# Optimization experiments

Hardware: AMD Instinct MI355X
Metric: run time of the kernel (lower is better)

Reference implementation:

```python
import jax, jax.numpy as jnp
import numpy as np

TOPK = 80
RADIUS_GAIN = 14.0
RADIUS_MIN = 1.5
RADIUS_MAX = 18.0
EPS = 1e-6


def _norm01(x, eps=EPS):
    # per-batch min/max normalization over all non-batch dims
    b = x.shape[0]
    flat = x.reshape(b, -1)
    mn = flat.min(axis=1).reshape(b, 1, 1, 1)
    mx = flat.max(axis=1).reshape(b, 1, 1, 1)
    return (x - mn) / (mx - mn + eps)


def _avg_pool(x, k):
    # torch avg_pool2d(kernel=k, stride=1, padding=k//2, count_include_pad=True)
    s = jax.lax.reduce_window(x, 0.0, jax.lax.add, (1, 1, k, k), (1, 1, 1, 1), 'SAME')
    return s / float(k * k)


def _max_pool(x, k):
    return jax.lax.reduce_window(x, -jnp.inf, jax.lax.max, (1, 1, k, k), (1, 1, 1, 1), 'SAME')


def _compact_connected_prior(score_map):
    occ = (score_map > 0.2).astype(score_map.dtype)
    local_occ = _avg_pool(occ, 9)
    local_mass = _avg_pool(score_map, 9)
    compact = _norm01(local_occ * local_mass)
    return score_map * compact


def _gaussian_map(score_map, depth):
    b, _, h, w = score_map.shape
    dtype = score_map.dtype
    pooled = _max_pool(score_map, 5)
    maxima = score_map * (score_map == pooled).astype(dtype)  # NMS keep local maxima

    flat = maxima.reshape(b, h * w)
    vals, inds = jax.lax.top_k(flat, TOPK)              # [B,K]
    vals = jnp.where(vals > 0, vals, jnp.zeros_like(vals))  # zero-weight masked peaks

    ys = (inds // w).astype(dtype)                       # [B,K]
    xs = (inds % w).astype(dtype)
    z = jnp.take_along_axis(depth.reshape(b, h * w), inds, axis=1)
    z = jnp.maximum(z, 1e-3)
    radius = jnp.clip(RADIUS_GAIN / z, RADIUS_MIN, RADIUS_MAX)
    sigma2 = (0.6 * radius) ** 2                         # [B,K]

    yy = jnp.arange(h, dtype=dtype)
    xx = jnp.arange(w, dtype=dtype)
    dx2 = (xx[None, None, None, :] - xs[:, :, None, None]) ** 2   # [B,K,1,W]
    dy2 = (yy[None, None, :, None] - ys[:, :, None, None]) ** 2   # [B,K,H,1]
    maps = vals[:, :, None, None] * jnp.exp(
        -(dx2 + dy2) / (2.0 * sigma2[:, :, None, None] + 1e-6))    # [B,K,H,W]
    gauss = maps.max(axis=1)[:, None]                    # [B,1,H,W]; maps>=0 so zero baseline preserved
    return _norm01(gauss)


def setup_inputs() -> dict:
    key = jax.random.key(0)
    k1, k2 = jax.random.split(key)
    B, H, W = 8, 320, 320
    voxel_score_map = jax.random.uniform(k1, (B, 1, H, W), dtype=jnp.float32)
    # depth within the module's valid z range [0.3, 20.0]
    depth = 0.3 + 19.7 * jax.random.uniform(k2, (B, 1, H, W), dtype=jnp.float32)
    return {'voxel_score_map': voxel_score_map, 'depth': depth}


def reference(voxel_score_map, depth):
    compact_score = _compact_connected_prior(voxel_score_map)
    return _gaussian_map(compact_score, depth)
```

## Files before the change

kernel.cpp:

```cpp
#include <hip/hip_runtime.h>
#include <math.h>

#define HH 320
#define WW 320
#define HWP (HH * WW)
#define KTOP 80
#define CNT_STRIDE 64
#define CAP (HWP / 2)
#define LVCAP 8192
#define TW 32
#define TH 64
#define NTPRX (WW / TW)
#define NTPI (NTPRX * (HH / TH))
#define GSW 64
#define GSH 16
#define SPRX (WW / GSW)
#define SPI (SPRX * (HH / GSH))
#define LOG2E 1.4426950408889634f
#define NLOG2TAU 19.931568569324174f

__device__ __forceinline__ void wave_minmax(float& mn, float& mx) {
    for (int off = 32; off > 0; off >>= 1) {
        mn = fminf(mn, __shfl_xor(mn, off, 64));
        mx = fmaxf(mx, __shfl_xor(mx, off, 64));
    }
}

__global__ __launch_bounds__(256) void pool_fused_k(
        const float* __restrict__ score, float* __restrict__ prod,
        float2* __restrict__ pmm, int* __restrict__ cand_cnt, int B_) {
    int tid = threadIdx.x;
    if (blockIdx.x == 0)
        for (int t = tid; t < B_ * CNT_STRIDE; t += 256) cand_cnt[t] = 0;
    int blk = blockIdx.x;
    int b = blk / NTPI, t = blk % NTPI;
    int ty0 = (t / NTPRX) * TH, tx0 = (t % NTPRX) * TW;
    __shared__ float rss[TH + 8][TW + 4];
    __shared__ float rso[TH + 8][TW + 4];
    const float4* img4 = (const float4*)(score + b * HWP);
    for (int i = tid; i < (TH + 8) * (TW / 4); i += 256) {
        int r = i / (TW / 4), q = i % (TW / 4);
        int gy = ty0 - 4 + r;
        float o0=0,o1=0,o2=0,o3=0,p0=0,p1=0,p2=0,p3=0;
        if (gy >= 0 && gy < HH) {
            const float4* row4 = img4 + gy * (WW / 4);
            int gq = tx0 / 4 + q;
            float4 a = (gq > 0) ? row4[gq - 1] : make_float4(0,0,0,0);
            float4 bb = row4[gq];
            float4 c = (gq < WW / 4 - 1) ? row4[gq + 1] : make_float4(0,0,0,0);
            float w0=a.x,w1=a.y,w2=a.z,w3=a.w,w4=bb.x,w5=bb.y,w6=bb.z,w7=bb.w,w8=c.x,w9=c.y,w10=c.z,w11=c.w;
            float s = w0+w1+w2+w3+w4+w5+w6+w7+w8;
            o0=s; s+=w9-w0; o1=s; s+=w10-w1; o2=s; s+=w11-w2; o3=s;
            float c0=(w0>0.2f)?1.f:0.f, c1=(w1>0.2f)?1.f:0.f, c2=(w2>0.2f)?1.f:0.f, c3=(w3>0.2f)?1.f:0.f;
            float c4=(w4>0.2f)?1.f:0.f, c5=(w5>0.2f)?1.f:0.f, c6=(w6>0.2f)?1.f:0.f, c7=(w7>0.2f)?1.f:0.f;
            float c8=(w8>0.2f)?1.f:0.f, c9=(w9>0.2f)?1.f:0.f, c10=(w10>0.2f)?1.f:0.f, c11=(w11>0.2f)?1.f:0.f;
            float u = c0+c1+c2+c3+c4+c5+c6+c7+c8;
            p0=u; u+=c9-c0; p1=u; u+=c10-c1; p2=u; u+=c11-c2; p3=u;
        }
        *(float4*)&rss[r][q * 4] = make_float4(o0,o1,o2,o3);
        *(float4*)&rso[r][q * 4] = make_float4(p0,p1,p2,p3);
    }
    __syncthreads();
    float tmn = INFINITY, tmx = 0.f;
    const float inv81 = 1.0f / 81.0f;
    float4* pr4 = (float4*)(prod + b * HWP);
    for (int i = tid; i < TH * (TW / 4); i += 256) {
        int r = i / (TW / 4), q = i % (TW / 4);
        float sx=0,sy=0,sz=0,sw=0, ox=0,oy=0,oz=0,ow=0;
#pragma unroll
        for (int j = 0; j < 9; ++j) {
            float4 s = *(float4*)&rss[r + j][q * 4];
            float4 o = *(float4*)&rso[r + j][q * 4];
            sx+=s.x; sy+=s.y; sz+=s.z; sw+=s.w;
            ox+=o.x; oy+=o.y; oz+=o.z; ow+=o.w;
        }
        float px=(ox*inv81)*(sx*inv81), py=(oy*inv81)*(sy*inv81);
        float pz=(oz*inv81)*(sz*inv81), pw=(ow*inv81)*(sw*inv81);
        pr4[(ty0 + r) * (WW / 4) + tx0 / 4 + q] = make_float4(px,py,pz,pw);
        tmn = fminf(tmn, fminf(fminf(px,py), fminf(pz,pw)));
        tmx = fmaxf(tmx, fmaxf(fmaxf(px,py), fmaxf(pz,pw)));
    }
    wave_minmax(tmn, tmx);
    __shared__ float wmn[4], wmx[4];
    int w = tid >> 6;
    if ((tid & 63) == 0) { wmn[w] = tmn; wmx[w] = tmx; }
    __syncthreads();
    if (tid == 0)
        pmm[blk] = make_float2(fminf(fminf(wmn[0],wmn[1]), fminf(wmn[2],wmn[3])),
                               fmaxf(fmaxf(wmx[0],wmx[1]), fmaxf(wmx[2],wmx[3])));
}

__global__ __launch_bounds__(256) void cs_nms_k(
        const float* __restrict__ score, const float* __restrict__ prod,
        const float2* __restrict__ pmm, float* __restrict__ cand_base,
        int* __restrict__ cand_cnt) {
    int tid = threadIdx.x;
    int blk = blockIdx.x;
    int b = blk / NTPI, t = blk % NTPI;
    int ty0 = (t / NTPRX) * TH, tx0 = (t % NTPRX) * TW;
    float tmn = INFINITY, tmx = 0.f;
    if (tid < NTPI) { float2 e = pmm[b * NTPI + tid]; tmn = e.x; tmx = e.y; }
    wave_minmax(tmn, tmx);
    __shared__ float s_mn, s_inv;
    if (tid == 0) { s_mn = tmn; s_inv = 1.0f / (tmx - tmn + 1e-6f); }
    __shared__ float cs[TH + 4][TW + 8 + 4];
    __shared__ float rm[TH + 4][TW + 4];
    __syncthreads();
    float mn = s_mn, inv = s_inv;
    const float4* sc4 = (const float4*)(score + b * HWP);
    const float4* pr4 = (const float4*)(prod + b * HWP);
    for (int i = tid; i < (TH + 4) * 10; i += 256) {
        int r = i / 10, q = i % 10;
        int gy = ty0 - 2 + r;
        int gq = tx0 / 4 - 1 + q;
        float4 c4 = make_float4(0,0,0,0);
        if (gy >= 0 && gy < HH && gq >= 0 && gq < WW / 4) {
            float4 s4 = sc4[gy * (WW / 4) + gq];
            float4 p4 = pr4[gy * (WW / 4) + gq];
            c4.x = s4.x * ((p4.x - mn) * inv); c4.y = s4.y * ((p4.y - mn) * inv);
            c4.z = s4.z * ((p4.z - mn) * inv); c4.w = s4.w * ((p4.w - mn) * inv);
        }
        *(float4*)&cs[r][q * 4] = c4;
    }
    __syncthreads();
    for (int i = tid; i < (TH + 4) * (TW / 4); i += 256) {
        int r = i / (TW / 4), x = (i % (TW / 4)) * 4;
        float c0=cs[r][x+2], c1=cs[r][x+3], c2=cs[r][x+4], c3=cs[r][x+5];
        float c4v=cs[r][x+6], c5=cs[r][x+7], c6=cs[r][x+8], c7=cs[r][x+9];
        float m01=fmaxf(c0,c1), m23=fmaxf(c2,c3), m45=fmaxf(c4v,c5), m67=fmaxf(c6,c7);
        float r0 = fmaxf(fmaxf(m01, m23), c4v);
        float r1 = fmaxf(fmaxf(c1, m23), m45);
        float r2 = fmaxf(fmaxf(m23, m45), c6);
        float r3 = fmaxf(fmaxf(c3, m45), m67);
        *(float4*)&rm[r][x] = make_float4(r0,r1,r2,r3);
    }
    __syncthreads();
    bool cd[8]; float vv[8]; int pb[2]; int offs[8];
#pragma unroll
    for (int qq = 0; qq < 2; ++qq) {
        int quad = qq * 256 + tid;
        int r = quad >> 3, x = (quad & 7) * 4;
        float4 v = *(float4*)&cs[r + 2][x + 4];
        float4 nm = *(float4*)&rm[r][x];
#pragma unroll
        for (int k = 1; k <= 4; ++k) {
            float4 rr = *(float4*)&rm[r + k][x];
            nm.x=fmaxf(nm.x,rr.x); nm.y=fmaxf(nm.y,rr.y);
            nm.z=fmaxf(nm.z,rr.z); nm.w=fmaxf(nm.w,rr.w);
        }
        pb[qq] = (ty0 + r) * WW + tx0 + x;
        cd[qq*4+0] = v.x > 0.f && v.x >= nm.x; vv[qq*4+0] = v.x;
        cd[qq*4+1] = v.y > 0.f && v.y >= nm.y; vv[qq*4+1] = v.y;
        cd[qq*4+2] = v.z > 0.f && v.z >= nm.z; vv[qq*4+2] = v.z;
        cd[qq*4+3] = v.w > 0.f && v.w >= nm.w; vv[qq*4+3] = v.w;
    }
    int lane = tid & 63, w = tid >> 6;
    unsigned long long lower = (1ULL << lane) - 1ULL;
    int wave_run = 0;
#pragma unroll
    for (int j = 0; j < 8; ++j) {
        unsigned long long m = __ballot(cd[j]);
        offs[j] = wave_run + __popcll(m & lower);
        wave_run += __popcll(m);
    }
    __shared__ int wbase[4];
    __shared__ int blockbase;
    if (lane == 0) wbase[w] = wave_run;
    __syncthreads();
    if (tid == 0) {
        int a0=wbase[0], a1=wbase[1], a2=wbase[2], a3=wbase[3];
        int tot = a0+a1+a2+a3;
        wbase[0]=0; wbase[1]=a0; wbase[2]=a0+a1; wbase[3]=a0+a1+a2;
        blockbase = tot ? atomicAdd(&cand_cnt[b * CNT_STRIDE], tot) : 0;
    }
    __syncthreads();
    float* cv = cand_base + b * HWP;
    int* ci = (int*)(cand_base + b * HWP + CAP);
    int bb2 = blockbase + wbase[w];
#pragma unroll
    for (int j = 0; j < 8; ++j) {
        if (cd[j]) {
            int slot = bb2 + offs[j];
            if (slot < CAP) { cv[slot] = vv[j]; ci[slot] = pb[j >> 2] + (j & 3); }
        }
    }
}

__global__ __launch_bounds__(1024) void topk_k(
        const float* __restrict__ cand_base, const int* __restrict__ cand_cnt,
        const float* __restrict__ depth, float4* __restrict__ pk4g) {
    int b = blockIdx.x;
    int tid = threadIdx.x;
    int n = cand_cnt[b * CNT_STRIDE];
    if (n > CAP) n = CAP;
    const float* cv = cand_base + b * HWP;
    const int* ci = (const int*)(cand_base + b * HWP + CAP);

    __shared__ float cvl[LVCAP];
    __shared__ int hist[256];
    __shared__ unsigned s_prefix;
    __shared__ int s_kth;
    __shared__ float sel_v[KTOP];
    __shared__ int sel_i[KTOP];
    __shared__ int s_ng, s_nt;
    __shared__ int tie_i[512];
    __shared__ float s_lvoff;

    bool inl = (n <= LVCAP);
    if (inl) {
        int n4 = n >> 2;
        const float4* cv4 = (const float4*)cv;
        for (int i = tid; i < n4; i += 1024) {
            float4 v = cv4[i];
            cvl[i*4+0] = v.x; cvl[i*4+1] = v.y; cvl[i*4+2] = v.z; cvl[i*4+3] = v.w;
        }
        for (int i = n4 * 4 + tid; i < n; i += 1024) cvl[i] = cv[i];
    }
    if (tid == 0) { s_prefix = 0; s_kth = KTOP; s_ng = 0; s_nt = 0; }
    if (tid < KTOP) { sel_v[tid] = 0.f; sel_i[tid] = -1; }
    __syncthreads();

    if (n > KTOP) {
        for (int shift = 24; shift >= 0; shift -= 8) {
            if (tid < 256) hist[tid] = 0;
            __syncthreads();
            unsigned pref = s_prefix;
            unsigned hmask = (shift == 24) ? 0u : (0xFFFFFFFFu << (shift + 8));
            for (int i = tid; i < n; i += 1024) {
                unsigned u = __float_as_uint(inl ? cvl[i] : cv[i]);
                if ((u & hmask) == (pref & hmask))
                    atomicAdd(&hist[(u >> shift) & 255], 1);
            }
            __syncthreads();
            if (tid < 64) {
                int h0 = hist[tid*4+0], h1 = hist[tid*4+1], h2 = hist[tid*4+2], h3 = hist[tid*4+3];
                int ls3 = h3, ls2 = h2 + ls3, ls1 = h1 + ls2, ls0 = h0 + ls1;
                int sum = ls0;
                for (int off = 1; off < 64; off <<= 1) {
                    int vv2 = __shfl_down(sum, off, 64);
                    if (tid + off < 64) sum += vv2;
                }
                int excl = sum - ls0;
                int kth = s_kth;
                int SS0=ls0+excl, SS1=ls1+excl, SS2=ls2+excl, SS3=ls3+excl, SS4=excl;
                unsigned pr = s_prefix;
                int bin = -1, rem = 0;
                if (SS0 >= kth && SS1 < kth) { bin = tid*4+0; rem = kth - SS1; }
                else if (SS1 >= kth && SS2 < kth) { bin = tid*4+1; rem = kth - SS2; }
                else if (SS2 >= kth && SS3 < kth) { bin = tid*4+2; rem = kth - SS3; }
                else if (SS3 >= kth && SS4 < kth) { bin = tid*4+3; rem = kth - SS4; }
                if (bin >= 0) { s_prefix = pr | ((unsigned)bin << shift); s_kth = rem; }
            }
            __syncthreads();
        }
        unsigned T = s_prefix;
        int need_eq = s_kth;
        for (int i = tid; i < n; i += 1024) {
            unsigned u = __float_as_uint(inl ? cvl[i] : cv[i]);
            if (u > T) {
                int s2 = atomicAdd(&s_ng, 1);
                if (s2 < KTOP) { sel_v[s2] = __uint_as_float(u); sel_i[s2] = ci[i]; }
            } else if (u == T) {
                int s2 = atomicAdd(&s_nt, 1);
                if (s2 < 512) tie_i[s2] = ci[i];
            }
        }
        __syncthreads();
        int G = s_ng; if (G > KTOP) G = KTOP;
        int nt = s_nt; if (nt > 512) nt = 512;
        for (int t2 = tid; t2 < nt; t2 += 1024) {
            int mine = tie_i[t2];
            int rank = 0;
            for (int j = 0; j < nt; ++j)
                if (tie_i[j] < mine) rank++;
            if (rank < need_eq && G + rank < KTOP) {
                sel_v[G + rank] = __uint_as_float(T);
                sel_i[G + rank] = mine;
            }
        }
        __syncthreads();
    } else {
        for (int i = tid; i < n; i += 1024) { sel_v[i] = cv[i]; sel_i[i] = ci[i]; }
        __syncthreads();
    }

    if (tid < 64) {
        float vmv = sel_v[tid];
        if (tid + 64 < KTOP) vmv = fmaxf(vmv, sel_v[tid + 64]);
        for (int off = 32; off > 0; off >>= 1) vmv = fmaxf(vmv, __shfl_xor(vmv, off, 64));
        if (tid == 0) s_lvoff = log2f(vmv + 1e-6f);
    }
    __syncthreads();

    if (tid < KTOP) {
        float val = sel_v[tid];
        int idx = sel_i[tid];
        float xk = 0.f, yk = 0.f, wv = -1.f, lv = -INFINITY;
        if (val > 0.f && idx >= 0) {
            yk = (float)(idx / WW);
            xk = (float)(idx % WW);
            float z = fmaxf(depth[b * HWP + idx], 1e-3f);
            float r = fminf(fmaxf(14.0f / z, 1.5f), 18.0f);
            float s2 = 0.6f * r;
            s2 = s2 * s2;
            wv = -LOG2E / (2.0f * s2 + 1e-6f);
            lv = log2f(val) - s_lvoff;
        }
        pk4g[b * KTOP + tid] = make_float4(lv, xk, yk, wv);
    }
}

__global__ __launch_bounds__(256) void gauss_out_k(const float4* __restrict__ pk4g,
                                                   float* __restrict__ out) {
    int blk = blockIdx.x, tid = threadIdx.x;
    int b = blk / SPI, s = blk % SPI;
    int sy = s / SPRX, sx = s % SPRX;
    int y0 = sy * GSH, x0 = sx * GSW;
    __shared__ float4 spk[KTOP];
    __shared__ int s_c0, s_cnt;
    bool keep = false;
    float4 pk;
    if (tid < KTOP) {
        pk = pk4g[b * KTOP + tid];
        float cut = (pk.x + NLOG2TAU) / (-pk.w);
        float rx0 = (float)x0, rx1 = (float)(x0 + GSW - 1);
        float ry0 = (float)y0, ry1 = (float)(y0 + GSH - 1);
        float cx = fminf(fmaxf(pk.y, rx0), rx1);
        float cy = fminf(fmaxf(pk.z, ry0), ry1);
        float dx = pk.y - cx, dy = pk.z - cy;
        keep = (dx * dx + dy * dy) <= cut;
    }
    int lane = tid & 63, w = tid >> 6;
    unsigned long long m = __ballot(keep);
    if (w == 0 && lane == 0) s_c0 = __popcll(m);
    __syncthreads();
    int base = (w == 0) ? 0 : s_c0;
    if (keep) spk[base + __popcll(m & ((1ULL << lane) - 1ULL))] = pk;
    if (w == 1 && lane == 0) s_cnt = s_c0 + __popcll(m);
    __syncthreads();
    int cnt = s_cnt;
    int r = tid >> 4, qx = tid & 15;
    int y = y0 + r, x = x0 + qx * 4;
    float fx = (float)x, fy = (float)y;
    float m0 = 0.f, m1 = 0.f, m2 = 0.f, m3 = 0.f;
    for (int i = 0; i < cnt; ++i) {
        float4 p = spk[i];
        float dy = fy - p.z;
        float dy2 = dy * dy;
        float dx0 = fx - p.y;
        float dx1 = dx0 + 1.f, dx2 = dx0 + 2.f, dx3 = dx0 + 3.f;
        m0 = fmaxf(m0, __builtin_amdgcn_exp2f(fmaf(fmaf(dx0, dx0, dy2), p.w, p.x)));
        m1 = fmaxf(m1, __builtin_amdgcn_exp2f(fmaf(fmaf(dx1, dx1, dy2), p.w, p.x)));
        m2 = fmaxf(m2, __builtin_amdgcn_exp2f(fmaf(fmaf(dx2, dx2, dy2), p.w, p.x)));
        m3 = fmaxf(m3, __builtin_amdgcn_exp2f(fmaf(fmaf(dx3, dx3, dy2), p.w, p.x)));
    }
    *(float4*)&out[b * HWP + y * WW + x] = make_float4(m0, m1, m2, m3);
}

extern "C" void kernel_launch(void* const* d_in, const int* in_sizes, int n_in,
                              void* d_out, int out_size, void* d_ws, size_t ws_size,
                              hipStream_t stream) {
    const float* score = (const float*)d_in[0];
    const float* depth = (const float*)d_in[1];
    float* out = (float*)d_out;
    int total = in_sizes[0];
    int B_ = total / HWP;

    float* buf1 = (float*)d_ws;
    float* buf2 = buf1 + total;
    char* small = (char*)(buf2 + total);
    float4* pk4 = (float4*)small;
    int* cand_cnt = (int*)(small + B_ * KTOP * sizeof(float4));
    float2* pmm = (float2*)(cand_cnt + B_ * CNT_STRIDE);

    pool_fused_k<<<B_ * NTPI, 256, 0, stream>>>(score, buf1, pmm, cand_cnt, B_);
    cs_nms_k<<<B_ * NTPI, 256, 0, stream>>>(score, buf1, pmm, buf2, cand_cnt);
    topk_k<<<B_, 1024, 0, stream>>>(buf2, cand_cnt, depth, pk4);
    gauss_out_k<<<B_ * SPI, 256, 0, stream>>>(pk4, out);
}
```

Before: 32.27 us.

## Fuse top-k selection into NMS kernel via last-block-done atomic counter

Merges the separate top-k kernel into the candidate-compaction kernel. Each batch's tiles increment a done counter, and the last tile to finish runs the radix top-k using 256 threads instead of 1024. Candidate stores and loads use agent-scope relaxed atomics so the last block sees the other blocks' writes. This removes one kernel launch and its gap, but the top-k now runs with a quarter of the threads and the coherent loads may be slower.

```diff
diff --git a/kernel.cpp b/kernel.cpp
--- a/kernel.cpp
+++ b/kernel.cpp
@@ -19,6 +19,9 @@
 #define LOG2E 1.4426950408889634f
 #define NLOG2TAU 19.931568569324174f
 
+#define STORE_COH(p, v) __hip_atomic_store((p), (v), __ATOMIC_RELAXED, __HIP_MEMORY_SCOPE_AGENT)
+#define LOAD_COH(p)     __hip_atomic_load((p), __ATOMIC_RELAXED, __HIP_MEMORY_SCOPE_AGENT)
+
 __device__ __forceinline__ void wave_minmax(float& mn, float& mx) {
     for (int off = 32; off > 0; off >>= 1) {
         mn = fminf(mn, __shfl_xor(mn, off, 64));
@@ -28,10 +31,11 @@
 
 __global__ __launch_bounds__(256) void pool_fused_k(
         const float* __restrict__ score, float* __restrict__ prod,
-        float2* __restrict__ pmm, int* __restrict__ cand_cnt, int B_) {
+        float2* __restrict__ pmm, int* __restrict__ cand_cnt,
+        int* __restrict__ done_cnt, int B_) {
     int tid = threadIdx.x;
     if (blockIdx.x == 0)
-        for (int t = tid; t < B_ * CNT_STRIDE; t += 256) cand_cnt[t] = 0;
+        for (int t = tid; t < B_ * CNT_STRIDE; t += 256) { cand_cnt[t] = 0; done_cnt[t] = 0; }
     int blk = blockIdx.x;
     int b = blk / NTPI, t = blk % NTPI;
     int ty0 = (t / NTPRX) * TH, tx0 = (t % NTPRX) * TW;
@@ -90,10 +94,11 @@
                                fmaxf(fmaxf(wmx[0],wmx[1]), fmaxf(wmx[2],wmx[3])));
 }
 
-__global__ __launch_bounds__(256) void cs_nms_k(
+__global__ __launch_bounds__(256) void cs_nms_topk_k(
         const float* __restrict__ score, const float* __restrict__ prod,
         const float2* __restrict__ pmm, float* __restrict__ cand_base,
-        int* __restrict__ cand_cnt) {
+        int* __restrict__ cand_cnt, int* __restrict__ done_cnt,
+        const float* __restrict__ depth, float4* __restrict__ pk4g) {
     int tid = threadIdx.x;
     int blk = blockIdx.x;
     int b = blk / NTPI, t = blk % NTPI;
@@ -174,24 +179,27 @@
         blockbase = tot ? atomicAdd(&cand_cnt[b * CNT_STRIDE], tot) : 0;
     }
     __syncthreads();
-    float* cv = cand_base + b * HWP;
-    int* ci = (int*)(cand_base + b * HWP + CAP);
+    float* cv_w = cand_base + b * HWP;
+    int* ci_w = (int*)(cand_base + b * HWP + CAP);
     int bb2 = blockbase + wbase[w];
 #pragma unroll
     for (int j = 0; j < 8; ++j) {
         if (cd[j]) {
             int slot = bb2 + offs[j];
-            if (slot < CAP) { cv[slot] = vv[j]; ci[slot] = pb[j >> 2] + (j & 3); }
-        }
-    }
-}
-
-__global__ __launch_bounds__(1024) void topk_k(
-        const float* __restrict__ cand_base, const int* __restrict__ cand_cnt,
-        const float* __restrict__ depth, float4* __restrict__ pk4g) {
-    int b = blockIdx.x;
-    int tid = threadIdx.x;
-    int n = cand_cnt[b * CNT_STRIDE];
+            if (slot < CAP) {
+                STORE_COH(&cv_w[slot], vv[j]);
+                STORE_COH(&ci_w[slot], pb[j >> 2] + (j & 3));
+            }
+        }
+    }
+    asm volatile("s_waitcnt vmcnt(0)" ::: "memory");
+    __syncthreads();
+    __shared__ int s_last;
+    if (tid == 0) s_last = atomicAdd(&done_cnt[b * CNT_STRIDE], 1);
+    __syncthreads();
+    if (s_last != NTPI - 1) return;
+
+    int n = atomicAdd(&cand_cnt[b * CNT_STRIDE], 0);
     if (n > CAP) n = CAP;
     const float* cv = cand_base + b * HWP;
     const int* ci = (const int*)(cand_base + b * HWP + CAP);
@@ -207,27 +215,20 @@
     __shared__ float s_lvoff;
 
     bool inl = (n <= LVCAP);
-    if (inl) {
-        int n4 = n >> 2;
-        const float4* cv4 = (const float4*)cv;
-        for (int i = tid; i < n4; i += 1024) {
-            float4 v = cv4[i];
-            cvl[i*4+0] = v.x; cvl[i*4+1] = v.y; cvl[i*4+2] = v.z; cvl[i*4+3] = v.w;
-        }
-        for (int i = n4 * 4 + tid; i < n; i += 1024) cvl[i] = cv[i];
-    }
+    if (inl)
+        for (int i = tid; i < n; i += 256) cvl[i] = LOAD_COH(&cv[i]);
     if (tid == 0) { s_prefix = 0; s_kth = KTOP; s_ng = 0; s_nt = 0; }
     if (tid < KTOP) { sel_v[tid] = 0.f; sel_i[tid] = -1; }
     __syncthreads();
 
     if (n > KTOP) {
         for (int shift = 24; shift >= 0; shift -= 8) {
-            if (tid < 256) hist[tid] = 0;
+            hist[tid] = 0;
             __syncthreads();
             unsigned pref = s_prefix;
             unsigned hmask = (shift == 24) ? 0u : (0xFFFFFFFFu << (shift + 8));
-            for (int i = tid; i < n; i += 1024) {
-                unsigned u = __float_as_uint(inl ? cvl[i] : cv[i]);
+            for (int i = tid; i < n; i += 256) {
+                unsigned u = __float_as_uint(inl ? cvl[i] : LOAD_COH(&cv[i]));
                 if ((u & hmask) == (pref & hmask))
                     atomicAdd(&hist[(u >> shift) & 255], 1);
             }
@@ -255,20 +256,20 @@
         }
         unsigned T = s_prefix;
         int need_eq = s_kth;
-        for (int i = tid; i < n; i += 1024) {
-            unsigned u = __float_as_uint(inl ? cvl[i] : cv[i]);
+        for (int i = tid; i < n; i += 256) {
+            unsigned u = __float_as_uint(inl ? cvl[i] : LOAD_COH(&cv[i]));
             if (u > T) {
                 int s2 = atomicAdd(&s_ng, 1);
-                if (s2 < KTOP) { sel_v[s2] = __uint_as_float(u); sel_i[s2] = ci[i]; }
+                if (s2 < KTOP) { sel_v[s2] = __uint_as_float(u); sel_i[s2] = LOAD_COH(&ci[i]); }
             } else if (u == T) {
                 int s2 = atomicAdd(&s_nt, 1);
-                if (s2 < 512) tie_i[s2] = ci[i];
+                if (s2 < 512) tie_i[s2] = LOAD_COH(&ci[i]);
             }
         }
         __syncthreads();
         int G = s_ng; if (G > KTOP) G = KTOP;
         int nt = s_nt; if (nt > 512) nt = 512;
-        for (int t2 = tid; t2 < nt; t2 += 1024) {
+        for (int t2 = tid; t2 < nt; t2 += 256) {
             int mine = tie_i[t2];
             int rank = 0;
             for (int j = 0; j < nt; ++j)
@@ -280,7 +281,7 @@
         }
         __syncthreads();
     } else {
-        for (int i = tid; i < n; i += 1024) { sel_v[i] = cv[i]; sel_i[i] = ci[i]; }
+        for (int i = tid; i < n; i += 256) { sel_v[i] = LOAD_COH(&cv[i]); sel_i[i] = LOAD_COH(&ci[i]); }
         __syncthreads();
     }
 
@@ -371,10 +372,11 @@
     char* small = (char*)(buf2 + total);
     float4* pk4 = (float4*)small;
     int* cand_cnt = (int*)(small + B_ * KTOP * sizeof(float4));
-    float2* pmm = (float2*)(cand_cnt + B_ * CNT_STRIDE);
-
-    pool_fused_k<<<B_ * NTPI, 256, 0, stream>>>(score, buf1, pmm, cand_cnt, B_);
-    cs_nms_k<<<B_ * NTPI, 256, 0, stream>>>(score, buf1, pmm, buf2, cand_cnt);
-    topk_k<<<B_, 1024, 0, stream>>>(buf2, cand_cnt, depth, pk4);
+    int* done_cnt = cand_cnt + B_ * CNT_STRIDE;
+    float2* pmm = (float2*)(done_cnt + B_ * CNT_STRIDE);
+
+    pool_fused_k<<<B_ * NTPI, 256, 0, stream>>>(score, buf1, pmm, cand_cnt, done_cnt, B_);
+    cs_nms_topk_k<<<B_ * NTPI, 256, 0, stream>>>(score, buf1, pmm, buf2, cand_cnt,
+                                                 done_cnt, depth, pk4);
     gauss_out_k<<<B_ * SPI, 256, 0, stream>>>(pk4, out);
 }
```

After: 43.88 us. +35.9%, slower.
